# Optimization experiments

Measured on AMD Instinct MI355X. Metric: run time of the kernel, lower is better.

## Reference

```python
import jax, jax.numpy as jnp
import numpy as np

B, S, D = 1, 4096, 1024
H = 16
HD = D // H  # 64
ROPE_THETA = 10000.0
NEG_INF = -1e9


def setup_inputs() -> dict:
    key = jax.random.key(0)
    ks = jax.random.split(key, 6)
    x = jax.random.normal(ks[0], (B, S, D), dtype=jnp.float32)
    # rotary frequencies: freqs_cis = exp(i * t * theta^{-2j/hd}), j in [0, hd/2)
    inv_freq = 1.0 / (ROPE_THETA ** (jnp.arange(0, HD, 2, dtype=jnp.float32) / HD))  # [HD/2]
    angles = jnp.arange(S, dtype=jnp.float32)[:, None] * inv_freq[None, :]  # [S, HD/2]
    freqs_cos = jnp.cos(angles)
    freqs_sin = jnp.sin(angles)
    # causal additive mask [S, S]
    mask = jnp.where(jnp.triu(jnp.ones((S, S), dtype=bool), k=1), NEG_INF, 0.0).astype(jnp.float32)
    scale = 0.02
    wq = jax.random.normal(ks[1], (D, D), dtype=jnp.float32) * scale
    wk = jax.random.normal(ks[2], (D, D), dtype=jnp.float32) * scale
    wv = jax.random.normal(ks[3], (D, D), dtype=jnp.float32) * scale
    wo = jax.random.normal(ks[4], (D, D), dtype=jnp.float32) * scale
    return {"x": x, "freqs_cos": freqs_cos, "freqs_sin": freqs_sin, "mask": mask,
            "wq": wq, "wk": wk, "wv": wv, "wo": wo}


def _apply_rope(t, cos, sin):
    # t: [B, S, H, HD]; cos/sin: [S, HD/2] -> broadcast [1, S, 1, HD/2]
    tr = t.reshape(*t.shape[:-1], HD // 2, 2)
    te, to = tr[..., 0], tr[..., 1]
    c = cos[None, :, None, :]
    s = sin[None, :, None, :]
    # complex multiply (te + i*to) * (c + i*s)
    oe = te * c - to * s
    oo = te * s + to * c
    return jnp.stack([oe, oo], axis=-1).reshape(t.shape)


def reference(x, freqs_cos, freqs_sin, mask, wq, wk, wv, wo):
    b, s, d = x.shape
    q = (x @ wq.T).reshape(b, s, H, HD)
    k = (x @ wk.T).reshape(b, s, H, HD)
    v = (x @ wv.T).reshape(b, s, H, HD)
    q = _apply_rope(q, freqs_cos, freqs_sin)
    k = _apply_rope(k, freqs_cos, freqs_sin)
    # [B, H, S, HD]
    q = q.transpose(0, 2, 1, 3)
    k = k.transpose(0, 2, 1, 3)
    v = v.transpose(0, 2, 1, 3)
    scores = jnp.einsum('bhqd,bhkd->bhqk', q, k) / jnp.sqrt(jnp.float32(HD))
    scores = scores + mask[None, None, :, :]
    probs = jax.nn.softmax(scores.astype(jnp.float32), axis=-1).astype(q.dtype)
    out = jnp.einsum('bhqk,bhkd->bhqd', probs, v)
    out = out.transpose(0, 2, 1, 3).reshape(b, s, d)
    return out @ wo.T
```

## Files before the change

### kernel.cpp

```cpp
#include <hip/hip_runtime.h>
#include <stdint.h>

typedef _Float16 f16;
typedef _Float16 v2h __attribute__((ext_vector_type(2)));
typedef _Float16 v4h __attribute__((ext_vector_type(4)));
typedef _Float16 v8h __attribute__((ext_vector_type(8)));
typedef float    v4f __attribute__((ext_vector_type(4)));

#define SEQ 4096
#define NH  16
#define DM  1024
#define QSCALE 0.18033688011112042f
#define MBASE 8.0f

__device__ __forceinline__ float exp2_(float x) {
#if __has_builtin(__builtin_amdgcn_exp2f)
  return __builtin_amdgcn_exp2f(x);
#else
  return exp2f(x);
#endif
}

__device__ __forceinline__ void gload_lds16(const void* g, void* l) {
  __builtin_amdgcn_global_load_lds((const __attribute__((address_space(1))) void*)g,
                                   (__attribute__((address_space(3))) void*)l,
                                   16, 0, 0);
}

#define NX 4194304
#define NW 1048576
__global__ void convert_kernel(const float* __restrict__ x,
                               const float* __restrict__ wq, const float* __restrict__ wk,
                               const float* __restrict__ wv, const float* __restrict__ wo,
                               f16* __restrict__ xf, f16* __restrict__ W, f16* __restrict__ Wo) {
  size_t e = ((size_t)blockIdx.x * 256 + threadIdx.x) * 4;
  const float* src; f16* dst;
  if (e < (size_t)NX) { src = x + e; dst = xf + e; }
  else {
    size_t j = e - NX; int wi = (int)(j >> 20); size_t off = j & (NW - 1);
    src = (wi == 0 ? wq : wi == 1 ? wk : wi == 2 ? wv : wo) + off;
    dst = (wi < 3 ? W + (size_t)wi * NW : Wo) + off;
  }
  v4f v = *(const v4f*)src;
  v4h o = { (f16)v.x, (f16)v.y, (f16)v.z, (f16)v.w };
  *(v4h*)dst = o;
}

__global__ __launch_bounds__(256, 2) void gemm_qkv_kernel(const f16* __restrict__ A,
                                                          const f16* __restrict__ B,
                                                          const float* __restrict__ fc,
                                                          const float* __restrict__ fs,
                                                          f16* __restrict__ Qh,
                                                          f16* __restrict__ Kh,
                                                          f16* __restrict__ Vtmp) {
  const int K = 1024;
  __shared__ __align__(16) f16 As[128 * 64];
  __shared__ __align__(16) f16 Bs[128 * 64];
  const int t = threadIdx.x;
  const int w = t >> 6, l = t & 63, quad = l >> 4, l15 = l & 15;
  const int wm = w & 1, wn = w >> 1;
  const int bx = blockIdx.x;
  const int m0 = blockIdx.y * 128, n0 = bx * 128;

  v4f acc[4][4];
#pragma unroll
  for (int i = 0; i < 4; ++i)
#pragma unroll
    for (int j = 0; j < 4; ++j) acc[i][j] = v4f{0.f, 0.f, 0.f, 0.f};

  for (int kt = 0; kt < 16; ++kt) {
    __syncthreads();
#pragma unroll
    for (int i = 0; i < 4; ++i) {
      int c = i * 256 + t; int r = c >> 3, cc = c & 7; int sc = cc ^ (r & 7);
      gload_lds16(A + (size_t)(m0 + r) * K + kt * 64 + sc * 8, As + c * 8);
      gload_lds16(B + (size_t)(n0 + r) * K + kt * 64 + sc * 8, Bs + c * 8);
    }
    __syncthreads();
#pragma unroll
    for (int ks = 0; ks < 2; ++ks) {
      v8h af[4], bf[4];
#pragma unroll
      for (int i = 0; i < 4; ++i) {
        int ra = wm * 64 + i * 16 + l15;
        af[i] = *(const v8h*)(As + ra * 64 + (((ks * 4 + quad) ^ (ra & 7)) * 8));
        int rb = wn * 64 + i * 16 + l15;
        bf[i] = *(const v8h*)(Bs + rb * 64 + (((ks * 4 + quad) ^ (rb & 7)) * 8));
      }
#pragma unroll
      for (int i = 0; i < 4; ++i)
#pragma unroll
        for (int j = 0; j < 4; ++j)
          acc[i][j] = __builtin_amdgcn_mfma_f32_16x16x32_f16(af[i], bf[j], acc[i][j], 0, 0, 0);
    }
  }
  const int mat = bx >> 3;
  if (mat < 2) {
    f16* dst = (mat == 0) ? Qh : Kh;
    const int hh = (bx & 7) * 2 + wn;
#pragma unroll
    for (int j = 0; j < 4; ++j) {
      const int d = j * 16 + l15;
      const int i2 = d >> 1;
      const float sgnmul = (l15 & 1) ? 1.f : -1.f;
#pragma unroll
      for (int i = 0; i < 4; ++i) {
#pragma unroll
        for (int rg = 0; rg < 4; ++rg) {
          float own = acc[i][j][rg];
          float par = __shfl_xor(own, 1);
          int m = m0 + wm * 64 + i * 16 + quad * 4 + rg;
          float c = fc[m * 32 + i2], sn = fs[m * 32 + i2];
          if (mat == 0) { c *= QSCALE; sn *= QSCALE; }
          float out = own * c + par * (sn * sgnmul);
          dst[((size_t)(hh * 4096 + m)) * 64 + d] = (f16)out;
        }
      }
    }
  } else {
#pragma unroll
    for (int i = 0; i < 4; ++i) {
      int m = m0 + wm * 64 + i * 16 + quad * 4;
#pragma unroll
      for (int j = 0; j < 4; ++j) {
        int nf = (bx - 16) * 128 + wn * 64 + j * 16 + l15;
#pragma unroll
        for (int rg = 0; rg < 4; ++rg)
          Vtmp[(size_t)(m + rg) * 1024 + nf] = (f16)acc[i][j][rg];
      }
    }
  }
}

__global__ void vtrans_kernel(const f16* __restrict__ Vtmp, f16* __restrict__ Vt) {
  __shared__ __align__(16) f16 T[64][72];
  int h = blockIdx.x >> 6, sb = blockIdx.x & 63;
  int t = threadIdx.x, s0 = sb * 64;
#pragma unroll
  for (int i = 0; i < 2; ++i) {
    int r = i * 32 + (t >> 3), c8 = t & 7;
    *(v8h*)(&T[r][c8 * 8]) = *(const v8h*)(Vtmp + (size_t)(s0 + r) * 1024 + h * 64 + c8 * 8);
  }
  __syncthreads();
#pragma unroll
  for (int i = 0; i < 4; ++i) {
    int idx = i * 256 + t;
    int d = idx >> 4;
    int sq = (idx & 15) * 4;
    int g = sq >> 5;
    int s32 = sq & 31;
    int kap = ((s32 >> 2) & 3) * 8 + (s32 >> 4) * 4;
    v4h o = { T[sq + 0][d], T[sq + 1][d], T[sq + 2][d], T[sq + 3][d] };
    *(v4h*)(Vt + (size_t)(h * 64 + d) * 4096 + s0 + g * 32 + kap) = o;
  }
}

__global__ __launch_bounds__(256, 4) void flash_kernel(const f16* __restrict__ Qh,
                                                       const f16* __restrict__ Kh,
                                                       const f16* __restrict__ Vt,
                                                       f16* __restrict__ Opart,
                                                       float* __restrict__ Lpart) {
  __shared__ __align__(16) f16 SM[16384];
  f16* Ks = SM;
  f16* Vs = SM + 8192;
  const int h = blockIdx.x & 15;
  const int sr = 79 - ((int)blockIdx.x >> 4);
  int qb, sp, nsp;
  if (sr < 8)       { qb = sr; sp = 0; nsp = 1; }
  else if (sr < 24) { int j = sr - 8;  qb = 8  + (j >> 1); sp = j & 1; nsp = 2; }
  else if (sr < 48) { int j = sr - 24; int q3 = j / 3; qb = 16 + q3; sp = j - 3 * q3; nsp = 3; }
  else              { int j = sr - 48; qb = 24 + (j >> 2); sp = j & 3; nsp = 4; }
  const int S = 2 * qb + 2;
  const int lo = (sp * S) / nsp, hi = ((sp + 1) * S) / nsp - 1;

  const int t = threadIdx.x, w = t >> 6, l = t & 63, quad = l >> 4, l15 = l & 15;
  const int q0w = qb * 128 + w * 32;

  v8h qf[2][2];
#pragma unroll
  for (int qt = 0; qt < 2; ++qt)
#pragma unroll
    for (int ks = 0; ks < 2; ++ks)
      qf[qt][ks] = *(const v8h*)(Qh + ((size_t)(h * 4096 + q0w + qt * 16 + l15)) * 64 + ks * 32 + quad * 8);

  v4f av[2][4];
#pragma unroll
  for (int qt = 0; qt < 2; ++qt)
#pragma unroll
    for (int db = 0; db < 4; ++db) av[qt][db] = v4f{0.f, 0.f, 0.f, 0.f};
  float lrun[2] = { 0.f, 0.f };

  const int c0 = t, c1 = 256 + t;
  const int r0 = c0 >> 3, sc0 = (c0 & 7) ^ (r0 & 7);
  const int r1 = c1 >> 3, sc1 = (c1 & 7) ^ (r1 & 7);
  const f16* KhB = Kh + (size_t)h * 4096 * 64;
  const f16* VtB = Vt + (size_t)h * 64 * 4096;

  {
    int koff = lo * 64;
    f16* Kd = Ks + (lo & 1) * 4096;
    f16* Vd = Vs + (lo & 1) * 4096;
    gload_lds16(KhB + (size_t)(koff + r0) * 64 + sc0 * 8, Kd + c0 * 8);
    gload_lds16(KhB + (size_t)(koff + r1) * 64 + sc1 * 8, Kd + c1 * 8);
    gload_lds16(VtB + (size_t)r0 * 4096 + koff + sc0 * 8, Vd + c0 * 8);
    gload_lds16(VtB + (size_t)r1 * 4096 + koff + sc1 * 8, Vd + c1 * 8);
  }

  for (int kb = lo; kb <= hi; ++kb) {
    __syncthreads();
    if (kb < hi) {
      int nb = (kb + 1) & 1;
      int koff = (kb + 1) * 64;
      gload_lds16(KhB + (size_t)(koff + r0) * 64 + sc0 * 8, Ks + nb * 4096 + c0 * 8);
      gload_lds16(KhB + (size_t)(koff + r1) * 64 + sc1 * 8, Ks + nb * 4096 + c1 * 8);
      gload_lds16(VtB + (size_t)r0 * 4096 + koff + sc0 * 8, Vs + nb * 4096 + c0 * 8);
      gload_lds16(VtB + (size_t)r1 * 4096 + koff + sc1 * 8, Vs + nb * 4096 + c1 * 8);
    }
    if (kb * 64 > q0w + 31) continue;
    const f16* Kc = Ks + (kb & 1) * 4096;
    const f16* Vc = Vs + (kb & 1) * 4096;

    v8h kf[4][2];
#pragma unroll
    for (int kt = 0; kt < 4; ++kt)
#pragma unroll
      for (int ks = 0; ks < 2; ++ks) {
        int r = kt * 16 + l15;
        kf[kt][ks] = *(const v8h*)(Kc + r * 64 + (((ks * 4 + quad) ^ (r & 7)) * 8));
      }

#pragma unroll
    for (int qt = 0; qt < 2; ++qt) {
      int qtb = q0w + qt * 16;
      if (kb * 64 > qtb + 15) continue;
      v4f st[4];
#pragma unroll
      for (int kt = 0; kt < 4; ++kt) {
        v4f z = v4f{ -MBASE, -MBASE, -MBASE, -MBASE };
        z = __builtin_amdgcn_mfma_f32_16x16x32_f16(kf[kt][0], qf[qt][0], z, 0, 0, 0);
        st[kt] = __builtin_amdgcn_mfma_f32_16x16x32_f16(kf[kt][1], qf[qt][1], z, 0, 0, 0);
      }
      if (kb * 64 + 63 > qtb) {
        int qg = qtb + l15;
#pragma unroll
        for (int kt = 0; kt < 4; ++kt)
#pragma unroll
          for (int jj = 0; jj < 4; ++jj) {
            int kg = kb * 64 + kt * 16 + quad * 4 + jj;
            if (kg > qg) st[kt][jj] = -1e30f;
          }
      }
      v8h pg[2];
      float rs = 0.f;
#pragma unroll
      for (int kt = 0; kt < 4; ++kt)
#pragma unroll
        for (int jj = 0; jj < 4; ++jj) {
          float p = exp2_(st[kt][jj]);
          rs += p;
          pg[kt >> 1][(kt & 1) * 4 + jj] = (f16)p;
        }
      lrun[qt] += rs;
#pragma unroll
      for (int db = 0; db < 4; ++db) {
        int r = db * 16 + l15;
#pragma unroll
        for (int g = 0; g < 2; ++g) {
          v8h vf = *(const v8h*)(Vc + r * 64 + (((g * 4 + quad) ^ (r & 7)) * 8));
          av[qt][db] = __builtin_amdgcn_mfma_f32_16x16x32_f16(vf, pg[g], av[qt][db], 0, 0, 0);
        }
      }
    }
  }
  const size_t base = (size_t)(h * 80 + sr);
#pragma unroll
  for (int qt = 0; qt < 2; ++qt) {
    float lr = lrun[qt];
    lr += __shfl_xor(lr, 16);
    lr += __shfl_xor(lr, 32);
    int q = w * 32 + qt * 16 + l15;
    if (quad == 0) Lpart[base * 128 + q] = lr;
#pragma unroll
    for (int db = 0; db < 4; ++db) {
      v4h o = { (f16)av[qt][db][0], (f16)av[qt][db][1],
                (f16)av[qt][db][2], (f16)av[qt][db][3] };
      *(v4h*)(Opart + base * 8192 + (size_t)q * 64 + db * 16 + quad * 4) = o;
    }
  }
}

__global__ void combine_kernel(const f16* __restrict__ Opart, const float* __restrict__ Lpart,
                               f16* __restrict__ attn) {
  int qb = blockIdx.x, h = blockIdx.y;
  int nsp, base;
  if (qb < 8)       { nsp = 1; base = qb; }
  else if (qb < 16) { nsp = 2; base = 8 + 2 * (qb - 8); }
  else if (qb < 24) { nsp = 3; base = 24 + 3 * (qb - 16); }
  else              { nsp = 4; base = 48 + 4 * (qb - 24); }
  int t = threadIdx.x, q = t >> 1, dh = (t & 1) * 32;
  float l = 0.f;
  float o[32];
#pragma unroll
  for (int c = 0; c < 32; ++c) o[c] = 0.f;
  for (int s = 0; s < nsp; ++s) {
    size_t sb = (size_t)(h * 80 + base + s);
    const f16* P = Opart + sb * 8192 + q * 64 + dh;
#pragma unroll
    for (int c = 0; c < 4; ++c) {
      v8h v = *(const v8h*)(P + c * 8);
#pragma unroll
      for (int j = 0; j < 8; ++j) o[c * 8 + j] += (float)v[j];
    }
    l += Lpart[sb * 128 + q];
  }
  float inv = 1.f / l;
#pragma unroll
  for (int c = 0; c < 4; ++c) {
    v8h v;
#pragma unroll
    for (int j = 0; j < 8; ++j) v[j] = (f16)(o[c * 8 + j] * inv);
    *(v8h*)(attn + (size_t)(qb * 128 + q) * 1024 + h * 64 + dh + c * 8) = v;
  }
}

__global__ __launch_bounds__(256, 3) void gemm_out_kernel(const f16* __restrict__ A,
                                                          const f16* __restrict__ B,
                                                          float* __restrict__ C) {
  const int K = 1024, N = 1024;
  __shared__ __align__(16) f16 As[128 * 64];
  __shared__ __align__(16) f16 Bs[64 * 64];
  const int t = threadIdx.x;
  const int w = t >> 6, l = t & 63, quad = l >> 4, l15 = l & 15;
  const int wm = w & 1, wn = w >> 1;
  const int m0 = blockIdx.y * 128, n0 = blockIdx.x * 64;

  v4f acc[4][2];
#pragma unroll
  for (int i = 0; i < 4; ++i)
#pragma unroll
    for (int j = 0; j < 2; ++j) acc[i][j] = v4f{0.f, 0.f, 0.f, 0.f};

  for (int kt = 0; kt < 16; ++kt) {
    __syncthreads();
#pragma unroll
    for (int i = 0; i < 4; ++i) {
      int c = i * 256 + t; int r = c >> 3, cc = c & 7; int sc = cc ^ (r & 7);
      gload_lds16(A + (size_t)(m0 + r) * K + kt * 64 + sc * 8, As + c * 8);
    }
#pragma unroll
    for (int i = 0; i < 2; ++i) {
      int c = i * 256 + t; int r = c >> 3, cc = c & 7; int sc = cc ^ (r & 7);
      gload_lds16(B + (size_t)(n0 + r) * K + kt * 64 + sc * 8, Bs + c * 8);
    }
    __syncthreads();
#pragma unroll
    for (int ks = 0; ks < 2; ++ks) {
      v8h af[4], bf[2];
#pragma unroll
      for (int i = 0; i < 4; ++i) {
        int ra = wm * 64 + i * 16 + l15;
        af[i] = *(const v8h*)(As + ra * 64 + (((ks * 4 + quad) ^ (ra & 7)) * 8));
      }
#pragma unroll
      for (int j = 0; j < 2; ++j) {
        int rb = wn * 32 + j * 16 + l15;
        bf[j] = *(const v8h*)(Bs + rb * 64 + (((ks * 4 + quad) ^ (rb & 7)) * 8));
      }
#pragma unroll
      for (int i = 0; i < 4; ++i)
#pragma unroll
        for (int j = 0; j < 2; ++j)
          acc[i][j] = __builtin_amdgcn_mfma_f32_16x16x32_f16(af[i], bf[j], acc[i][j], 0, 0, 0);
    }
  }
#pragma unroll
  for (int i = 0; i < 4; ++i) {
    int m = m0 + wm * 64 + i * 16 + quad * 4;
#pragma unroll
    for (int j = 0; j < 2; ++j) {
      int n = n0 + wn * 32 + j * 16 + l15;
#pragma unroll
      for (int rg = 0; rg < 4; ++rg)
        C[(size_t)(m + rg) * N + n] = acc[i][j][rg];
    }
  }
}

extern "C" void kernel_launch(void* const* d_in, const int* in_sizes, int n_in,
                              void* d_out, int out_size, void* d_ws, size_t ws_size,
                              hipStream_t stream) {
  (void)in_sizes; (void)n_in; (void)out_size; (void)ws_size;
  const float* x  = (const float*)d_in[0];
  const float* fc = (const float*)d_in[1];
  const float* fs = (const float*)d_in[2];
  const float* wq = (const float*)d_in[4];
  const float* wk = (const float*)d_in[5];
  const float* wv = (const float*)d_in[6];
  const float* wo = (const float*)d_in[7];
  float* out = (float*)d_out;
  char* ws = (char*)d_ws;

  f16* xf    = (f16*)(ws);
  f16* W     = (f16*)(ws + 8388608);
  f16* Wo    = (f16*)(ws + 14680064);
  f16* Vtmp  = (f16*)(ws + 16777216);
  f16* Qh    = (f16*)(ws + 41943040);
  f16* Kh    = (f16*)(ws + 50331648);
  f16* Vt    = (f16*)(ws + 58720256);
  f16* attn  = xf;
  f16* Opart = Vtmp;
  float* Lpart = (float*)(ws + 16777216 + 20971520);

  convert_kernel<<<dim3(8192), dim3(256), 0, stream>>>(x, wq, wk, wv, wo, xf, W, Wo);
  gemm_qkv_kernel<<<dim3(24, 32), dim3(256), 0, stream>>>(xf, W, fc, fs, Qh, Kh, Vtmp);
  vtrans_kernel<<<dim3(1024), dim3(256), 0, stream>>>(Vtmp, Vt);
  flash_kernel<<<dim3(1280), dim3(256), 0, stream>>>(Qh, Kh, Vt, Opart, Lpart);
  combine_kernel<<<dim3(32, 16), dim3(256), 0, stream>>>(Opart, Lpart, attn);
  gemm_out_kernel<<<dim3(16, 32), dim3(256), 0, stream>>>(attn, Wo, out);
}
```

Measured before the change: 243.4 us.

## Fuse V transpose into QKV GEMM epilogue and compute row sums via MFMA

The separate vtrans kernel is removed. The QKV GEMM's V-output blocks now stage the accumulator tile in shared memory and write the transposed, permuted Vt layout directly, which drops one launch and the Vtmp round trip through global memory. In the flash kernel, the per-row probability sum is now computed by an extra MFMA against a ones vector instead of scalar adds and shuffles, and probabilities are packed with cvt_pkrtz. The risks are a larger LDS footprint in the GEMM and a change in rounding, since the sums are taken from the rounded f16 P values.

```diff
diff --git a/kernel.cpp b/kernel.cpp
--- a/kernel.cpp
+++ b/kernel.cpp
@@ -6,6 +6,7 @@
 typedef _Float16 v4h __attribute__((ext_vector_type(4)));
 typedef _Float16 v8h __attribute__((ext_vector_type(8)));
 typedef float    v4f __attribute__((ext_vector_type(4)));
+typedef __fp16   v2fp __attribute__((ext_vector_type(2)));
 
 #define SEQ 4096
 #define NH  16
@@ -19,6 +20,11 @@
 #else
   return exp2f(x);
 #endif
+}
+
+__device__ __forceinline__ v2h pkrtz(float a, float b) {
+  v2fp r = __builtin_amdgcn_cvt_pkrtz(a, b);
+  return __builtin_bit_cast(v2h, r);
 }
 
 __device__ __forceinline__ void gload_lds16(const void* g, void* l) {
@@ -52,10 +58,11 @@
                                                           const float* __restrict__ fs,
                                                           f16* __restrict__ Qh,
                                                           f16* __restrict__ Kh,
-                                                          f16* __restrict__ Vtmp) {
+                                                          f16* __restrict__ Vt) {
   const int K = 1024;
-  __shared__ __align__(16) f16 As[128 * 64];
-  __shared__ __align__(16) f16 Bs[128 * 64];
+  __shared__ __align__(16) f16 SM[16640];
+  f16* As = SM;
+  f16* Bs = SM + 8192;
   const int t = threadIdx.x;
   const int w = t >> 6, l = t & 63, quad = l >> 4, l15 = l & 15;
   const int wm = w & 1, wn = w >> 1;
@@ -118,40 +125,34 @@
       }
     }
   } else {
+    __syncthreads();
+    f16* T = SM;
 #pragma unroll
     for (int i = 0; i < 4; ++i) {
-      int m = m0 + wm * 64 + i * 16 + quad * 4;
+      int srow = wm * 64 + i * 16 + quad * 4;
 #pragma unroll
       for (int j = 0; j < 4; ++j) {
-        int nf = (bx - 16) * 128 + wn * 64 + j * 16 + l15;
+        int dd = wn * 64 + j * 16 + l15;
 #pragma unroll
         for (int rg = 0; rg < 4; ++rg)
-          Vtmp[(size_t)(m + rg) * 1024 + nf] = (f16)acc[i][j][rg];
-      }
-    }
-  }
-}
-
-__global__ void vtrans_kernel(const f16* __restrict__ Vtmp, f16* __restrict__ Vt) {
-  __shared__ __align__(16) f16 T[64][72];
-  int h = blockIdx.x >> 6, sb = blockIdx.x & 63;
-  int t = threadIdx.x, s0 = sb * 64;
-#pragma unroll
-  for (int i = 0; i < 2; ++i) {
-    int r = i * 32 + (t >> 3), c8 = t & 7;
-    *(v8h*)(&T[r][c8 * 8]) = *(const v8h*)(Vtmp + (size_t)(s0 + r) * 1024 + h * 64 + c8 * 8);
-  }
-  __syncthreads();
-#pragma unroll
-  for (int i = 0; i < 4; ++i) {
-    int idx = i * 256 + t;
-    int d = idx >> 4;
-    int sq = (idx & 15) * 4;
-    int g = sq >> 5;
-    int s32 = sq & 31;
-    int kap = ((s32 >> 2) & 3) * 8 + (s32 >> 4) * 4;
-    v4h o = { T[sq + 0][d], T[sq + 1][d], T[sq + 2][d], T[sq + 3][d] };
-    *(v4h*)(Vt + (size_t)(h * 64 + d) * 4096 + s0 + g * 32 + kap) = o;
+          T[(srow + rg) * 130 + dd] = (f16)acc[i][j][rg];
+      }
+    }
+    __syncthreads();
+    const int hv0 = (bx - 16) * 2;
+#pragma unroll
+    for (int loop = 0; loop < 16; ++loop) {
+      int flat = loop * 256 + t;
+      int dd = flat >> 5;
+      int rem = flat & 31;
+      int g = rem >> 3, kapc = rem & 7;
+      int q = kapc >> 1, b = kapc & 1;
+      int sb = g * 32 + 16 * b + 4 * q;
+      v4h v = { T[(sb + 0) * 130 + dd], T[(sb + 1) * 130 + dd],
+                T[(sb + 2) * 130 + dd], T[(sb + 3) * 130 + dd] };
+      int h = hv0 + (dd >> 6), d = dd & 63;
+      *(v4h*)(Vt + (size_t)(h * 64 + d) * 4096 + m0 + g * 32 + kapc * 4) = v;
+    }
   }
 }
 
@@ -183,12 +184,18 @@
     for (int ks = 0; ks < 2; ++ks)
       qf[qt][ks] = *(const v8h*)(Qh + ((size_t)(h * 4096 + q0w + qt * 16 + l15)) * 64 + ks * 32 + quad * 8);
 
+  v8h onesh;
+#pragma unroll
+  for (int j = 0; j < 8; ++j) onesh[j] = (f16)1.f;
+
   v4f av[2][4];
-#pragma unroll
-  for (int qt = 0; qt < 2; ++qt)
+  v4f avl[2];
+#pragma unroll
+  for (int qt = 0; qt < 2; ++qt) {
+    avl[qt] = v4f{0.f, 0.f, 0.f, 0.f};
 #pragma unroll
     for (int db = 0; db < 4; ++db) av[qt][db] = v4f{0.f, 0.f, 0.f, 0.f};
-  float lrun[2] = { 0.f, 0.f };
+  }
 
   const int c0 = t, c1 = 256 + t;
   const int r0 = c0 >> 3, sc0 = (c0 & 7) ^ (r0 & 7);
@@ -250,24 +257,24 @@
             if (kg > qg) st[kt][jj] = -1e30f;
           }
       }
-      v8h pg[2];
-      float rs = 0.f;
-#pragma unroll
-      for (int kt = 0; kt < 4; ++kt)
-#pragma unroll
-        for (int jj = 0; jj < 4; ++jj) {
-          float p = exp2_(st[kt][jj]);
-          rs += p;
-          pg[kt >> 1][(kt & 1) * 4 + jj] = (f16)p;
-        }
-      lrun[qt] += rs;
+      union { v8h v8[2]; v2h v2[8]; } P;
+#pragma unroll
+      for (int kt = 0; kt < 4; ++kt) {
+        float p0 = exp2_(st[kt][0]), p1 = exp2_(st[kt][1]);
+        float p2 = exp2_(st[kt][2]), p3 = exp2_(st[kt][3]);
+        P.v2[kt * 2 + 0] = pkrtz(p0, p1);
+        P.v2[kt * 2 + 1] = pkrtz(p2, p3);
+      }
+#pragma unroll
+      for (int g = 0; g < 2; ++g)
+        avl[qt] = __builtin_amdgcn_mfma_f32_16x16x32_f16(onesh, P.v8[g], avl[qt], 0, 0, 0);
 #pragma unroll
       for (int db = 0; db < 4; ++db) {
         int r = db * 16 + l15;
 #pragma unroll
         for (int g = 0; g < 2; ++g) {
           v8h vf = *(const v8h*)(Vc + r * 64 + (((g * 4 + quad) ^ (r & 7)) * 8));
-          av[qt][db] = __builtin_amdgcn_mfma_f32_16x16x32_f16(vf, pg[g], av[qt][db], 0, 0, 0);
+          av[qt][db] = __builtin_amdgcn_mfma_f32_16x16x32_f16(vf, P.v8[g], av[qt][db], 0, 0, 0);
         }
       }
     }
@@ -275,11 +282,8 @@
   const size_t base = (size_t)(h * 80 + sr);
 #pragma unroll
   for (int qt = 0; qt < 2; ++qt) {
-    float lr = lrun[qt];
-    lr += __shfl_xor(lr, 16);
-    lr += __shfl_xor(lr, 32);
     int q = w * 32 + qt * 16 + l15;
-    if (quad == 0) Lpart[base * 128 + q] = lr;
+    if (quad == 0) Lpart[base * 128 + q] = avl[qt][0];
 #pragma unroll
     for (int db = 0; db < 4; ++db) {
       v4h o = { (f16)av[qt][db][0], (f16)av[qt][db][1],
@@ -403,17 +407,15 @@
   f16* xf    = (f16*)(ws);
   f16* W     = (f16*)(ws + 8388608);
   f16* Wo    = (f16*)(ws + 14680064);
-  f16* Vtmp  = (f16*)(ws + 16777216);
+  f16* Opart = (f16*)(ws + 16777216);
+  float* Lpart = (float*)(ws + 16777216 + 20971520);
   f16* Qh    = (f16*)(ws + 41943040);
   f16* Kh    = (f16*)(ws + 50331648);
   f16* Vt    = (f16*)(ws + 58720256);
   f16* attn  = xf;
-  f16* Opart = Vtmp;
-  float* Lpart = (float*)(ws + 16777216 + 20971520);
 
   convert_kernel<<<dim3(8192), dim3(256), 0, stream>>>(x, wq, wk, wv, wo, xf, W, Wo);
-  gemm_qkv_kernel<<<dim3(24, 32), dim3(256), 0, stream>>>(xf, W, fc, fs, Qh, Kh, Vtmp);
-  vtrans_kernel<<<dim3(1024), dim3(256), 0, stream>>>(Vtmp, Vt);
+  gemm_qkv_kernel<<<dim3(24, 32), dim3(256), 0, stream>>>(xf, W, fc, fs, Qh, Kh, Vt);
   flash_kernel<<<dim3(1280), dim3(256), 0, stream>>>(Qh, Kh, Vt, Opart, Lpart);
   combine_kernel<<<dim3(32, 16), dim3(256), 0, stream>>>(Opart, Lpart, attn);
   gemm_out_kernel<<<dim3(16, 32), dim3(256), 0, stream>>>(attn, Wo, out);
```

New measurement: 237.6 us. -2.4%, faster.
